# Optimization experiments

Hardware: AMD Instinct MI355X
Metric: run time of the kernel (lower is better)

Reference implementation:

```python
import jax, jax.numpy as jnp
import numpy as np

N_THRESH = 100  # thresholds = 0.00, 0.01, ..., 0.99


def setup_inputs() -> dict:
    key = jax.random.key(0)
    k1, k2 = jax.random.split(key)
    predicted_mask = jax.random.uniform(k1, (32, 1, 1024, 1024), dtype=jnp.float32)
    gt_mask = jax.random.randint(k2, (32, 1, 1024, 1024), 0, 2, dtype=jnp.int32)
    return {"predicted_mask": predicted_mask, "gt_mask": gt_mask}


def reference(predicted_mask, gt_mask):
    # Single-pass histogram formulation of: for each t_k in arange(0,1,0.01),
    # iou_k = |(pred > t_k) & gt| / |(pred > t_k) | gt|  (torchmetrics binary Jaccard,
    # strict '>' thresholding, safe-divide -> 0 when union is empty).
    thresholds = jnp.arange(0.0, 1.0, 0.01, dtype=jnp.float32)  # [100], sorted
    pred = jnp.squeeze(predicted_mask).ravel()                  # [N] probabilities in [0,1]
    gt = jnp.squeeze(gt_mask).ravel().astype(jnp.float32)       # [N] 0/1

    # cnt[i] = number of thresholds strictly below pred[i]; pixel i satisfies
    # (pred > t_k) exactly for k in [0, cnt[i]).
    cnt = jnp.searchsorted(thresholds, pred, side='left')       # [N] int in [0, 100]

    hist_pos = jax.ops.segment_sum(gt, cnt, num_segments=N_THRESH + 1)              # [101]
    hist_all = jax.ops.segment_sum(jnp.ones_like(gt), cnt, num_segments=N_THRESH + 1)

    # TP_k = #{pred > t_k and gt==1} = sum_{c > k} hist_pos[c]  (suffix sums via cumsum)
    tp = jnp.sum(hist_pos) - jnp.cumsum(hist_pos)[:N_THRESH]        # [100]
    pred_pos = jnp.sum(hist_all) - jnp.cumsum(hist_all)[:N_THRESH]  # [100] #{pred > t_k}
    n_gt_pos = jnp.sum(gt)

    union = pred_pos + n_gt_pos - tp                                 # TP + FP + FN
    ious = jnp.where(union > 0, tp / jnp.maximum(union, 1.0), 0.0)   # safe divide -> 0
    return thresholds, ious
```

## Files before the change

kernel.cpp:

```cpp
#include <hip/hip_runtime.h>

#define N_THRESH 100
#define NBINS 101
#define COLS 32

__global__ void zero_ws_kernel(unsigned long long* __restrict__ ws) {
    int i = threadIdx.x;
    if (i < NBINS) ws[i] = 0ull;
}

__device__ __forceinline__ int bin_of(float v) {
    int e = (int)(v * 100.0f);
    e = e < 0 ? 0 : (e > 99 ? 99 : e);
    double ed = (double)e * 0.01;
    float t0 = (float)ed;
    float t1 = (float)(ed + 0.01);
    int c = e + (t0 < v ? 1 : 0) + (t1 < v ? 1 : 0);
    return c > N_THRESH ? N_THRESH : c;
}

__global__ __launch_bounds__(256) void hist_kernel(
        const float* __restrict__ pred,
        const int* __restrict__ gt,
        unsigned long long* __restrict__ ws,
        int n) {
    __shared__ unsigned int hist[NBINS][COLS];

    const int tid = threadIdx.x;
    const int col = tid & (COLS - 1);

    for (int i = tid; i < NBINS * COLS; i += 256)
        (&hist[0][0])[i] = 0u;
    __syncthreads();

    const int nvec = n >> 2;
    const float4* __restrict__ p4 = (const float4*)pred;
    const int4*   __restrict__ g4 = (const int4*)gt;
    const int gsz = gridDim.x * blockDim.x;

    int i = blockIdx.x * blockDim.x + tid;
    for (; i + 7 * gsz < nvec; i += 8 * gsz) {
        float4 p[8];
        int4   g[8];
#pragma unroll
        for (int u = 0; u < 8; ++u) {
            p[u] = p4[i + u * gsz];
            g[u] = g4[i + u * gsz];
        }
#pragma unroll
        for (int u = 0; u < 8; ++u) {
            atomicAdd(&hist[bin_of(p[u].x)][col],
                      1u | ((unsigned int)(g[u].x != 0) << 16));
            atomicAdd(&hist[bin_of(p[u].y)][col],
                      1u | ((unsigned int)(g[u].y != 0) << 16));
            atomicAdd(&hist[bin_of(p[u].z)][col],
                      1u | ((unsigned int)(g[u].z != 0) << 16));
            atomicAdd(&hist[bin_of(p[u].w)][col],
                      1u | ((unsigned int)(g[u].w != 0) << 16));
        }
    }
    for (; i < nvec; i += gsz) {
        float4 p = p4[i];
        int4   g = g4[i];
        atomicAdd(&hist[bin_of(p.x)][col], 1u | ((unsigned int)(g.x != 0) << 16));
        atomicAdd(&hist[bin_of(p.y)][col], 1u | ((unsigned int)(g.y != 0) << 16));
        atomicAdd(&hist[bin_of(p.z)][col], 1u | ((unsigned int)(g.z != 0) << 16));
        atomicAdd(&hist[bin_of(p.w)][col], 1u | ((unsigned int)(g.w != 0) << 16));
    }

    if (blockIdx.x == 0 && tid == 0) {
        for (int k = nvec << 2; k < n; ++k) {
            atomicAdd(&hist[bin_of(pred[k])][0],
                      1u | ((unsigned int)(gt[k] != 0) << 16));
        }
    }

    __syncthreads();
    if (tid < NBINS) {
        unsigned long long cnt = 0ull, pos = 0ull;
#pragma unroll
        for (int j = 0; j < COLS; ++j) {
            unsigned int v = hist[tid][(j + tid) & (COLS - 1)];
            cnt += v & 0xffffu;
            pos += v >> 16;
        }
        unsigned long long s = (pos << 32) | cnt;
        if (s) atomicAdd(&ws[tid], s);
    }
}

__global__ void finalize_kernel(const unsigned long long* __restrict__ ws,
                                float* __restrict__ out) {
    __shared__ unsigned int pos[NBINS], all[NBINS];
    int k = threadIdx.x;
    if (k < NBINS) {
        unsigned long long h = ws[k];
        pos[k] = (unsigned int)(h >> 32);
        all[k] = (unsigned int)(h & 0xffffffffull);
    }
    __syncthreads();
    if (k < N_THRESH) {
        out[k] = (float)((double)k * 0.01);
        unsigned long long tp = 0, pp = 0, ngt = 0;
        for (int c = k + 1; c <= N_THRESH; ++c) { tp += pos[c]; pp += all[c]; }
        for (int c = 0; c <= N_THRESH; ++c) ngt += pos[c];
        long long uni = (long long)(pp + ngt - tp);
        double iou = (uni > 0) ? (double)tp / (double)uni : 0.0;
        out[N_THRESH + k] = (float)iou;
    }
}

extern "C" void kernel_launch(void* const* d_in, const int* in_sizes, int n_in,
                              void* d_out, int out_size, void* d_ws, size_t ws_size,
                              hipStream_t stream) {
    const float* pred = (const float*)d_in[0];
    const int*   gt   = (const int*)d_in[1];
    float* out = (float*)d_out;
    unsigned long long* ws = (unsigned long long*)d_ws;
    int n = in_sizes[0];

    zero_ws_kernel<<<1, 128, 0, stream>>>(ws);
    hist_kernel<<<2048, 256, 0, stream>>>(pred, gt, ws, n);
    finalize_kernel<<<1, 128, 0, stream>>>(ws, out);
}
```

Measured before the change: 303.3 us.

## Replace shared atomics with per-thread private 8-bit packed histogram columns

Gives each thread its own column of 16-bit shared counters, with an 8-bit count and an 8-bit positive count, so updates are plain read-modify-write instead of LDS atomics. Every 63 iterations the block reduces the columns into registers and clears them, so the 8-bit fields cannot overflow. The grid drops to 768 blocks to amortise the periodic flush. The cost is extra syncs and reduction work per chunk, plus bank conflicts from data-dependent row indexing.

```diff
diff --git a/kernel.cpp b/kernel.cpp
--- a/kernel.cpp
+++ b/kernel.cpp
@@ -2,7 +2,8 @@
 
 #define N_THRESH 100
 #define NBINS 101
-#define COLS 32
+#define TPB 256
+#define CHUNK 63
 
 __global__ void zero_ws_kernel(unsigned long long* __restrict__ ws) {
     int i = threadIdx.x;
@@ -19,71 +20,106 @@
     return c > N_THRESH ? N_THRESH : c;
 }
 
-__global__ __launch_bounds__(256) void hist_kernel(
+__device__ __forceinline__ void bump(unsigned short (*h)[TPB], int tid, float v, int g) {
+    h[bin_of(v)][tid] += (unsigned short)(1u + (g != 0 ? 256u : 0u));
+}
+
+__global__ __launch_bounds__(TPB) void hist_kernel(
         const float* __restrict__ pred,
         const int* __restrict__ gt,
         unsigned long long* __restrict__ ws,
         int n) {
-    __shared__ unsigned int hist[NBINS][COLS];
+    __shared__ unsigned short h[NBINS][TPB];
 
     const int tid = threadIdx.x;
-    const int col = tid & (COLS - 1);
 
-    for (int i = tid; i < NBINS * COLS; i += 256)
-        (&hist[0][0])[i] = 0u;
+    for (int i = tid; i < NBINS * (TPB / 2); i += TPB)
+        ((unsigned int*)h)[i] = 0u;
     __syncthreads();
 
     const int nvec = n >> 2;
     const float4* __restrict__ p4 = (const float4*)pred;
     const int4*   __restrict__ g4 = (const int4*)gt;
     const int gsz = gridDim.x * blockDim.x;
+    const int i0  = blockIdx.x * blockDim.x + tid;
+    const int iters = (nvec + gsz - 1) / gsz;
 
-    int i = blockIdx.x * blockDim.x + tid;
-    for (; i + 7 * gsz < nvec; i += 8 * gsz) {
-        float4 p[8];
-        int4   g[8];
-#pragma unroll
-        for (int u = 0; u < 8; ++u) {
-            p[u] = p4[i + u * gsz];
-            g[u] = g4[i + u * gsz];
+    unsigned long long acc_cnt = 0ull, acc_pos = 0ull;
+
+    int it = 0;
+    for (;;) {
+        const int cap = min(iters, it + CHUNK);
+        for (; it + 4 <= cap; it += 4) {
+            const int i = i0 + it * gsz;
+            if (i + 3 * gsz < nvec) {
+                float4 pa = p4[i];           int4 ga = g4[i];
+                float4 pb = p4[i + gsz];     int4 gb = g4[i + gsz];
+                float4 pc = p4[i + 2 * gsz]; int4 gc = g4[i + 2 * gsz];
+                float4 pd = p4[i + 3 * gsz]; int4 gd = g4[i + 3 * gsz];
+                bump(h, tid, pa.x, ga.x); bump(h, tid, pa.y, ga.y);
+                bump(h, tid, pa.z, ga.z); bump(h, tid, pa.w, ga.w);
+                bump(h, tid, pb.x, gb.x); bump(h, tid, pb.y, gb.y);
+                bump(h, tid, pb.z, gb.z); bump(h, tid, pb.w, gb.w);
+                bump(h, tid, pc.x, gc.x); bump(h, tid, pc.y, gc.y);
+                bump(h, tid, pc.z, gc.z); bump(h, tid, pc.w, gc.w);
+                bump(h, tid, pd.x, gd.x); bump(h, tid, pd.y, gd.y);
+                bump(h, tid, pd.z, gd.z); bump(h, tid, pd.w, gd.w);
+            } else {
+                for (int u = 0; u < 4; ++u) {
+                    int ii = i + u * gsz;
+                    if (ii < nvec) {
+                        float4 p = p4[ii]; int4 g = g4[ii];
+                        bump(h, tid, p.x, g.x); bump(h, tid, p.y, g.y);
+                        bump(h, tid, p.z, g.z); bump(h, tid, p.w, g.w);
+                    }
+                }
+            }
         }
-#pragma unroll
-        for (int u = 0; u < 8; ++u) {
-            atomicAdd(&hist[bin_of(p[u].x)][col],
-                      1u | ((unsigned int)(g[u].x != 0) << 16));
-            atomicAdd(&hist[bin_of(p[u].y)][col],
-                      1u | ((unsigned int)(g[u].y != 0) << 16));
-            atomicAdd(&hist[bin_of(p[u].z)][col],
-                      1u | ((unsigned int)(g[u].z != 0) << 16));
-            atomicAdd(&hist[bin_of(p[u].w)][col],
-                      1u | ((unsigned int)(g[u].w != 0) << 16));
+        for (; it < cap; ++it) {
+            int i = i0 + it * gsz;
+            if (i < nvec) {
+                float4 p = p4[i]; int4 g = g4[i];
+                bump(h, tid, p.x, g.x); bump(h, tid, p.y, g.y);
+                bump(h, tid, p.z, g.z); bump(h, tid, p.w, g.w);
+            }
         }
-    }
-    for (; i < nvec; i += gsz) {
-        float4 p = p4[i];
-        int4   g = g4[i];
-        atomicAdd(&hist[bin_of(p.x)][col], 1u | ((unsigned int)(g.x != 0) << 16));
-        atomicAdd(&hist[bin_of(p.y)][col], 1u | ((unsigned int)(g.y != 0) << 16));
-        atomicAdd(&hist[bin_of(p.z)][col], 1u | ((unsigned int)(g.z != 0) << 16));
-        atomicAdd(&hist[bin_of(p.w)][col], 1u | ((unsigned int)(g.w != 0) << 16));
+        if (it >= iters) break;
+
+        __syncthreads();
+        if (tid < NBINS) {
+            unsigned int c = 0, p = 0;
+            const unsigned int* row = (const unsigned int*)&h[tid][0];
+            for (int j = 0; j < TPB / 2; ++j) {
+                unsigned int v = row[(j + tid) & (TPB / 2 - 1)];
+                c += (v & 0xffu) + ((v >> 16) & 0xffu);
+                p += ((v >> 8) & 0xffu) + ((v >> 24) & 0xffu);
+            }
+            acc_cnt += c; acc_pos += p;
+        }
+        __syncthreads();
+        for (int i = tid; i < NBINS * (TPB / 2); i += TPB)
+            ((unsigned int*)h)[i] = 0u;
+        __syncthreads();
     }
 
     if (blockIdx.x == 0 && tid == 0) {
         for (int k = nvec << 2; k < n; ++k) {
-            atomicAdd(&hist[bin_of(pred[k])][0],
-                      1u | ((unsigned int)(gt[k] != 0) << 16));
+            int b = bin_of(pred[k]);
+            h[b][0] = (unsigned short)(h[b][0] + (1u + (gt[k] != 0 ? 256u : 0u)));
         }
     }
 
     __syncthreads();
     if (tid < NBINS) {
-        unsigned long long cnt = 0ull, pos = 0ull;
-#pragma unroll
-        for (int j = 0; j < COLS; ++j) {
-            unsigned int v = hist[tid][(j + tid) & (COLS - 1)];
-            cnt += v & 0xffffu;
-            pos += v >> 16;
+        unsigned int c = 0, p = 0;
+        const unsigned int* row = (const unsigned int*)&h[tid][0];
+        for (int j = 0; j < TPB / 2; ++j) {
+            unsigned int v = row[(j + tid) & (TPB / 2 - 1)];
+            c += (v & 0xffu) + ((v >> 16) & 0xffu);
+            p += ((v >> 8) & 0xffu) + ((v >> 24) & 0xffu);
         }
+        unsigned long long cnt = acc_cnt + c;
+        unsigned long long pos = acc_pos + p;
         unsigned long long s = (pos << 32) | cnt;
         if (s) atomicAdd(&ws[tid], s);
     }
@@ -120,6 +156,6 @@
     int n = in_sizes[0];
 
     zero_ws_kernel<<<1, 128, 0, stream>>>(ws);
-    hist_kernel<<<2048, 256, 0, stream>>>(pred, gt, ws, n);
+    hist_kernel<<<768, TPB, 0, stream>>>(pred, gt, ws, n);
     finalize_kernel<<<1, 128, 0, stream>>>(ws, out);
 }
```

Result: faster. 294.2 us (-3.0%).

## Use per-thread private 8-bit packed LDS histograms and fuse finalize via last-block

Applied to the files above, without the earlier changes.

Replaces shared-memory atomics on a 32-column histogram with per-thread private histogram columns of 16-bit cells, each packing an 8-bit count and an 8-bit positive count, split across two LDS arrays. Blocks periodically fold and clear the arrays to avoid 8-bit overflow, and software-prefetch the next group of loads. The separate finalize kernel is removed: the last block to finish, detected with an atomic counter, computes the IoU outputs. This drops LDS atomic contention and one launch, at the cost of large LDS use (about 155KB), lower occupancy and periodic fold/zero barriers.

```diff
diff --git a/kernel.cpp b/kernel.cpp
--- a/kernel.cpp
+++ b/kernel.cpp
@@ -2,11 +2,13 @@
 
 #define N_THRESH 100
 #define NBINS 101
-#define COLS 32
+#define TPB 384
+#define GRID 1024
+#define FLUSH_GROUPS 29
 
 __global__ void zero_ws_kernel(unsigned long long* __restrict__ ws) {
     int i = threadIdx.x;
-    if (i < NBINS) ws[i] = 0ull;
+    if (i < NBINS + 1) ws[i] = 0ull;
 }
 
 __device__ __forceinline__ int bin_of(float v) {
@@ -19,94 +21,141 @@
     return c > N_THRESH ? N_THRESH : c;
 }
 
-__global__ __launch_bounds__(256) void hist_kernel(
+__device__ __forceinline__ void bump(unsigned short* h, int tid, float v, int g) {
+    h[bin_of(v) * TPB + tid] += (unsigned short)(1u + (g != 0 ? 256u : 0u));
+}
+
+__device__ __forceinline__ void fold_row(const unsigned short* h, int r,
+                                         unsigned long long& acc_c,
+                                         unsigned long long& acc_p) {
+    const unsigned int* row = (const unsigned int*)(h + r * TPB);
+    unsigned int c = 0, p = 0;
+    for (int j = 0; j < TPB / 2; ++j) {
+        int jj = j + r; if (jj >= TPB / 2) jj -= TPB / 2;
+        unsigned int v = row[jj];
+        c += (v & 0xffu) + ((v >> 16) & 0xffu);
+        p += ((v >> 8) & 0xffu) + ((v >> 24) & 0xffu);
+    }
+    acc_c += c; acc_p += p;
+}
+
+#define PROCESS16(PA, PB, PC, PD, GA, GB, GC, GD) do {            \
+    bump(sA, tid, (PA).x, (GA).x); bump(sB, tid, (PA).y, (GA).y); \
+    bump(sA, tid, (PA).z, (GA).z); bump(sB, tid, (PA).w, (GA).w); \
+    bump(sA, tid, (PB).x, (GB).x); bump(sB, tid, (PB).y, (GB).y); \
+    bump(sA, tid, (PB).z, (GB).z); bump(sB, tid, (PB).w, (GB).w); \
+    bump(sA, tid, (PC).x, (GC).x); bump(sB, tid, (PC).y, (GC).y); \
+    bump(sA, tid, (PC).z, (GC).z); bump(sB, tid, (PC).w, (GC).w); \
+    bump(sA, tid, (PD).x, (GD).x); bump(sB, tid, (PD).y, (GD).y); \
+    bump(sA, tid, (PD).z, (GD).z); bump(sB, tid, (PD).w, (GD).w); \
+} while (0)
+
+__global__ __launch_bounds__(TPB) void hist_kernel(
         const float* __restrict__ pred,
         const int* __restrict__ gt,
         unsigned long long* __restrict__ ws,
+        float* __restrict__ out,
         int n) {
-    __shared__ unsigned int hist[NBINS][COLS];
+    __shared__ unsigned short sA[NBINS * TPB];
+    __shared__ unsigned short sB[NBINS * TPB];
+    __shared__ unsigned int fpos[NBINS], fall[NBINS];
+    __shared__ int is_last;
 
     const int tid = threadIdx.x;
-    const int col = tid & (COLS - 1);
+    unsigned int* const za = (unsigned int*)sA;
+    unsigned int* const zb = (unsigned int*)sB;
 
-    for (int i = tid; i < NBINS * COLS; i += 256)
-        (&hist[0][0])[i] = 0u;
+    for (int i = tid; i < NBINS * (TPB / 2); i += TPB) { za[i] = 0u; zb[i] = 0u; }
     __syncthreads();
 
     const int nvec = n >> 2;
     const float4* __restrict__ p4 = (const float4*)pred;
     const int4*   __restrict__ g4 = (const int4*)gt;
     const int gsz = gridDim.x * blockDim.x;
+    const int i0  = blockIdx.x * blockDim.x + tid;
+    const int iters  = nvec / gsz;
+    const int groups = iters >> 2;
 
-    int i = blockIdx.x * blockDim.x + tid;
-    for (; i + 7 * gsz < nvec; i += 8 * gsz) {
-        float4 p[8];
-        int4   g[8];
-#pragma unroll
-        for (int u = 0; u < 8; ++u) {
-            p[u] = p4[i + u * gsz];
-            g[u] = g4[i + u * gsz];
+    unsigned long long acc_c = 0ull, acc_p = 0ull;
+
+    int gs = 0;
+    while (gs < groups) {
+        const int ge = (groups < gs + FLUSH_GROUPS) ? groups : gs + FLUSH_GROUPS;
+        int j = i0 + gs * 4 * gsz;
+        float4 pa = p4[j], pb = p4[j + gsz], pc = p4[j + 2 * gsz], pd = p4[j + 3 * gsz];
+        int4   ga = g4[j], gb = g4[j + gsz], gc = g4[j + 2 * gsz], gd = g4[j + 3 * gsz];
+        for (int g = gs + 1; g < ge; ++g) {
+            j = i0 + g * 4 * gsz;
+            float4 qa = p4[j], qb = p4[j + gsz], qc = p4[j + 2 * gsz], qd = p4[j + 3 * gsz];
+            int4   ra = g4[j], rb = g4[j + gsz], rc = g4[j + 2 * gsz], rd = g4[j + 3 * gsz];
+            PROCESS16(pa, pb, pc, pd, ga, gb, gc, gd);
+            pa = qa; pb = qb; pc = qc; pd = qd;
+            ga = ra; gb = rb; gc = rc; gd = rd;
         }
-#pragma unroll
-        for (int u = 0; u < 8; ++u) {
-            atomicAdd(&hist[bin_of(p[u].x)][col],
-                      1u | ((unsigned int)(g[u].x != 0) << 16));
-            atomicAdd(&hist[bin_of(p[u].y)][col],
-                      1u | ((unsigned int)(g[u].y != 0) << 16));
-            atomicAdd(&hist[bin_of(p[u].z)][col],
-                      1u | ((unsigned int)(g[u].z != 0) << 16));
-            atomicAdd(&hist[bin_of(p[u].w)][col],
-                      1u | ((unsigned int)(g[u].w != 0) << 16));
+        PROCESS16(pa, pb, pc, pd, ga, gb, gc, gd);
+        gs = ge;
+        if (gs < groups) {
+            __syncthreads();
+            if (tid < NBINS)                            fold_row(sA, tid, acc_c, acc_p);
+            else if (tid >= 192 && tid < 192 + NBINS)   fold_row(sB, tid - 192, acc_c, acc_p);
+            __syncthreads();
+            for (int i = tid; i < NBINS * (TPB / 2); i += TPB) { za[i] = 0u; zb[i] = 0u; }
+            __syncthreads();
         }
     }
-    for (; i < nvec; i += gsz) {
-        float4 p = p4[i];
-        int4   g = g4[i];
-        atomicAdd(&hist[bin_of(p.x)][col], 1u | ((unsigned int)(g.x != 0) << 16));
-        atomicAdd(&hist[bin_of(p.y)][col], 1u | ((unsigned int)(g.y != 0) << 16));
-        atomicAdd(&hist[bin_of(p.z)][col], 1u | ((unsigned int)(g.z != 0) << 16));
-        atomicAdd(&hist[bin_of(p.w)][col], 1u | ((unsigned int)(g.w != 0) << 16));
+
+    for (int k = groups * 4; ; ++k) {
+        int i = i0 + k * gsz;
+        if (i >= nvec) break;
+        float4 p = p4[i]; int4 g = g4[i];
+        bump(sA, tid, p.x, g.x); bump(sB, tid, p.y, g.y);
+        bump(sA, tid, p.z, g.z); bump(sB, tid, p.w, g.w);
     }
 
     if (blockIdx.x == 0 && tid == 0) {
         for (int k = nvec << 2; k < n; ++k) {
-            atomicAdd(&hist[bin_of(pred[k])][0],
-                      1u | ((unsigned int)(gt[k] != 0) << 16));
+            int b = bin_of(pred[k]);
+            sA[b * TPB] = (unsigned short)(sA[b * TPB] + 1u + (gt[k] != 0 ? 256u : 0u));
         }
     }
 
     __syncthreads();
-    if (tid < NBINS) {
-        unsigned long long cnt = 0ull, pos = 0ull;
-#pragma unroll
-        for (int j = 0; j < COLS; ++j) {
-            unsigned int v = hist[tid][(j + tid) & (COLS - 1)];
-            cnt += v & 0xffffu;
-            pos += v >> 16;
-        }
-        unsigned long long s = (pos << 32) | cnt;
-        if (s) atomicAdd(&ws[tid], s);
-    }
-}
-
-__global__ void finalize_kernel(const unsigned long long* __restrict__ ws,
-                                float* __restrict__ out) {
-    __shared__ unsigned int pos[NBINS], all[NBINS];
-    int k = threadIdx.x;
-    if (k < NBINS) {
-        unsigned long long h = ws[k];
-        pos[k] = (unsigned int)(h >> 32);
-        all[k] = (unsigned int)(h & 0xffffffffull);
+    if (tid >= 192 && tid < 192 + NBINS) {
+        fold_row(sB, tid - 192, acc_c, acc_p);
+        fall[tid - 192] = (unsigned int)acc_c;
+        fpos[tid - 192] = (unsigned int)acc_p;
     }
     __syncthreads();
-    if (k < N_THRESH) {
-        out[k] = (float)((double)k * 0.01);
-        unsigned long long tp = 0, pp = 0, ngt = 0;
-        for (int c = k + 1; c <= N_THRESH; ++c) { tp += pos[c]; pp += all[c]; }
-        for (int c = 0; c <= N_THRESH; ++c) ngt += pos[c];
-        long long uni = (long long)(pp + ngt - tp);
-        double iou = (uni > 0) ? (double)tp / (double)uni : 0.0;
-        out[N_THRESH + k] = (float)iou;
+    if (tid < NBINS) {
+        fold_row(sA, tid, acc_c, acc_p);
+        unsigned long long cnt = acc_c + fall[tid];
+        unsigned long long pos = acc_p + fpos[tid];
+        if (cnt | pos) atomicAdd(&ws[tid], (pos << 32) | cnt);
+        __threadfence();
+    }
+    __syncthreads();
+    if (tid == 0) {
+        unsigned long long t = atomicAdd(&ws[NBINS], 1ull);
+        is_last = (t == (unsigned long long)(gridDim.x - 1)) ? 1 : 0;
+    }
+    __syncthreads();
+
+    if (is_last) {
+        if (tid < NBINS) {
+            unsigned long long h = atomicAdd(&ws[tid], 0ull);
+            fpos[tid] = (unsigned int)(h >> 32);
+            fall[tid] = (unsigned int)(h & 0xffffffffull);
+        }
+        __syncthreads();
+        if (tid < N_THRESH) {
+            out[tid] = (float)((double)tid * 0.01);
+            unsigned long long tp = 0, pp = 0, ngt = 0;
+            for (int c = tid + 1; c <= N_THRESH; ++c) { tp += fpos[c]; pp += fall[c]; }
+            for (int c = 0; c <= N_THRESH; ++c) ngt += fpos[c];
+            long long uni = (long long)(pp + ngt - tp);
+            double iou = (uni > 0) ? (double)tp / (double)uni : 0.0;
+            out[N_THRESH + tid] = (float)iou;
+        }
     }
 }
 
@@ -120,6 +169,5 @@
     int n = in_sizes[0];
 
     zero_ws_kernel<<<1, 128, 0, stream>>>(ws);
-    hist_kernel<<<2048, 256, 0, stream>>>(pred, gt, ws, n);
-    finalize_kernel<<<1, 128, 0, stream>>>(ws, out);
+    hist_kernel<<<GRID, TPB, 0, stream>>>(pred, gt, ws, out, n);
 }
```

Result: slower. 352.4 us (+16.2%).
